# Optimization experiments

Hardware: AMD Instinct MI355X
Metric: run time of the kernel (lower is better)

Reference implementation:

```python
import jax, jax.numpy as jnp
import numpy as np

# 4D conv over (L, P, W, H) decomposed as k shifted 3D convs over (P, W, H),
# with the L spatial dim folded into the batch. Faithful to convNd(num_dims=4),
# stride 1, 'same' padding (padding = (k-1)//2), no bias.

def conv4d(x, w):
    # x: [B, C, L, P, W, H]; w: [O, I, k, k, k, k]
    k = w.shape[2]
    p = (k - 1) // 2
    B, C, L, P, Wd, Hd = x.shape
    O = w.shape[0]
    xp = jnp.pad(x, ((0, 0), (0, 0), (p, p), (0, 0), (0, 0), (0, 0)))
    dn = ('NCDHW', 'OIDHW', 'NCDHW')
    out = jnp.zeros((B, O, L, P, Wd, Hd), x.dtype)
    for dl in range(k):  # k <= 3, static loop over kernel taps along L
        xs = xp[:, :, dl:dl + L]                                  # [B,C,L,P,W,H]
        xs = xs.transpose(0, 2, 1, 3, 4, 5).reshape(B * L, C, P, Wd, Hd)
        y = jax.lax.conv_general_dilated(xs, w[:, :, dl], (1, 1, 1),
                                         [(p, p)] * 3, dimension_numbers=dn)
        out = out + y.reshape(B, L, O, P, Wd, Hd).transpose(0, 2, 1, 3, 4, 5)
    return out


def inception4d(x, weights):
    # mean over parallel 4D convs with kernel sizes 1, 3, ... (2i+1)
    acc = conv4d(x, weights[0])
    for w in weights[1:]:
        acc = acc + conv4d(x, w)
    return acc / len(weights)


def setup_inputs() -> dict:
    key = jax.random.key(0)
    ks = jax.random.split(key, 5)
    B, T, W, H, C = 4, 48, 8, 8, 32
    d_model, d_ff = 32, 64
    x = jax.random.normal(ks[0], (B, T, W, H, C), dtype=jnp.float32)
    # Inception_Block4D weights: kernel sizes 1 and 3 (num_kernels=2), no bias
    w1_0 = jax.random.normal(ks[1], (d_ff, d_model, 1, 1, 1, 1), dtype=jnp.float32) * 0.1
    w1_1 = jax.random.normal(ks[2], (d_ff, d_model, 3, 3, 3, 3), dtype=jnp.float32) * 0.02
    w2_0 = jax.random.normal(ks[3], (d_model, d_ff, 1, 1, 1, 1), dtype=jnp.float32) * 0.1
    w2_1 = jax.random.normal(ks[4], (d_model, d_ff, 3, 3, 3, 3), dtype=jnp.float32) * 0.02
    return {"x": x, "w1_0": w1_0, "w1_1": w1_1, "w2_0": w2_0, "w2_1": w2_1}


def reference(x, w1_0, w1_1, w2_0, w2_1):
    B, T, W, H, C = x.shape
    periods = (2, 3, 4)                       # FFT_for_Period hardcoded output
    xf = jnp.ones((B, len(periods)), x.dtype) # hardcoded uniform weights
    real_len = T                              # seq_len + pred_len
    res = []
    for period in periods:
        if real_len % period != 0:
            length = (real_len // period + 1) * period
            out = jnp.concatenate([x, x[:, -(length - real_len):]], axis=1)
        else:
            length = real_len
            out = x
        # [B, L, P, W, H, C] -> [B, C, L, P, W, H]
        out = out.reshape(B, length // period, period, W, H, C).transpose(0, 5, 1, 2, 3, 4)
        h = inception4d(out, [w1_0, w1_1])
        h = jax.nn.gelu(h, approximate=False)  # torch nn.GELU default (exact)
        h = inception4d(h, [w2_0, w2_1])
        # [B, C, L, P, W, H] -> [B, (L P), W, H, C]
        h = h.transpose(0, 2, 3, 4, 5, 1).reshape(B, length, W, H, C)
        res.append(h[:, :real_len])
    res = jnp.stack(res, axis=1)              # [B, k, T, W, H, C]
    pw = jax.nn.softmax(xf, axis=1).reshape(B, len(periods), 1, 1, 1, 1)
    return jnp.sum(res * pw, axis=1) + x
```

## Files before the change

### kernel.cpp

```cpp
#include <hip/hip_runtime.h>
#include <math.h>


typedef __attribute__((ext_vector_type(8))) short bf16x8;
typedef __attribute__((ext_vector_type(4))) float f32x4;
typedef unsigned short u16;

#define XC 3200
#define HC 6400
#define XSEG 617600
#define ZSEG_END 636800
#define W1OFF 636800
#define W2OFF 802688
#define H1OFF 968576
#define H1P 1235200
#define PREP_N 1300352
#define OUT_Q 98304
#define PREP_TOT (PREP_N + OUT_Q)

#define WAITVM(N) asm volatile("s_waitcnt vmcnt(" #N ")" ::: "memory")
#define SBAR()    asm volatile("s_barrier" ::: "memory")

__device__ __forceinline__ u16 f2bf(float f) {
    unsigned u = __float_as_uint(f);
    unsigned r = u + 0x7fffu + ((u >> 16) & 1u);
    return (u16)(r >> 16);
}
__device__ __forceinline__ float gelu_exact(float v) {
    return 0.5f * v * (1.0f + erff(v * 0.7071067811865476f));
}

__device__ __forceinline__ void cp1k(const u16* g, u16* l, int lane) {
    __builtin_amdgcn_global_load_lds(
        (const __attribute__((address_space(1))) unsigned int*)(g + lane * 8),
        (__attribute__((address_space(3))) unsigned int*)(l + lane * 8),
        16, 0, 0);
}

__global__ __launch_bounds__(256) void prep(
    const float* __restrict__ x,
    const float* __restrict__ w1_0, const float* __restrict__ w1_1,
    const float* __restrict__ w2_0, const float* __restrict__ w2_1,
    u16* __restrict__ ws, float* __restrict__ out) {
    int i = blockIdx.x * 256 + threadIdx.x;
    if (i < XSEG) {
        int cellidx = i / XC; int inner = i - cellidx * XC;
        int cellpos = inner >> 5; int low = inner & 31;
        int sc = low >> 3, jj = low & 7;
        int c = ((sc ^ (cellpos & 3)) << 3) + jj;
        int wp = cellpos / 10, hp = cellpos - (cellpos / 10) * 10;
        float v = 0.f;
        if (cellidx < 192 && wp >= 1 && wp <= 8 && hp >= 1 && hp <= 8)
            v = x[(cellidx * 64 + (wp - 1) * 8 + (hp - 1)) * 32 + c];
        ws[i] = f2bf(v);
    } else if (i < ZSEG_END) {
        int j = i - XSEG;
        int per = j / HC; int off = j - per * HC;
        ws[H1OFF + per * H1P + 192 * HC + off] = 0;
    } else if (i < ZSEG_END + 165888) {
        int j = i - W1OFF;
        int tap = j >> 11; int r = j & 2047;
        int chunk = r >> 3, jj = r & 7;
        int m = chunk & 15, nt = (chunk >> 4) & 3, quad = chunk >> 6;
        int o = nt * 16 + m, c = quad * 8 + jj;
        float v = 0.5f * w1_1[(o * 32 + c) * 81 + tap];
        if (tap == 40) v += 0.5f * w1_0[o * 32 + c];
        ws[i] = f2bf(v);
    } else if (i < PREP_N) {
        int j = i - W2OFF;
        int tap = j >> 11; int r = j & 2047;
        int chunk = r >> 3, jj = r & 7;
        int m = chunk & 15, nt = (chunk >> 4) & 1;
        int quad = (chunk >> 5) & 3, ks = chunk >> 7;
        int o = nt * 16 + m, c = ks * 32 + quad * 8 + jj;
        float v = 0.5f * w2_1[(o * 64 + c) * 81 + tap];
        if (tap == 40) v += 0.5f * w2_0[o * 64 + c];
        ws[i] = f2bf(v);
    } else if (i < PREP_TOT) {
        int j = i - PREP_N;
        ((float4*)out)[j] = ((const float4*)x)[j];
    }
}

template<int P>
__device__ __forceinline__ int cidx(int bb, int l2, int q2) {
    constexpr int L = 48 / P;
    return ((unsigned)l2 < (unsigned)L && (unsigned)q2 < (unsigned)P)
               ? bb * 48 + l2 * P + q2 : 192;
}

template<int P>
__device__ __forceinline__ void conv1_body(
    const u16* __restrict__ xs, const u16* __restrict__ w1b,
    u16* __restrict__ h1, int tp, int bb,
    u16* __restrict__ s_w, u16* __restrict__ s_a) {
    constexpr int HB = (P == 2) ? 0 : (P == 3) ? H1P : 2 * H1P;

    int tid = threadIdx.x;
    int lane = tid & 63, wv = tid >> 6;
    int m = lane & 15, quad = lane >> 4;
    int tloc = wv >> 1, nh = wv & 1;

    int t0 = tp * 2, t1 = tp * 2 + 1;
    int l0 = t0 / P, q0 = t0 - l0 * P;
    int l1 = t1 / P, q1 = t1 - l1 * P;

    int sp[4];
#pragma unroll
    for (int mt = 0; mt < 4; ++mt) {
        int pos = mt * 16 + m;
        sp[mt] = (pos >> 3) * 10 + (pos & 7);
    }

    f32x4 acc[4][2];
#pragma unroll
    for (int mt = 0; mt < 4; ++mt)
#pragma unroll
        for (int nt = 0; nt < 2; ++nt) acc[mt][nt] = f32x4{0.f, 0.f, 0.f, 0.f};

    auto stageW = [&](int cgn) {
        const u16* src = w1b + (cgn * 3) * 2048;
        u16* dst = s_w + (cgn & 3) * 6144;
        int p0 = wv * 3;
#pragma unroll
        for (int i = 0; i < 3; ++i)
            cp1k(src + (p0 + i) * 512, dst + (p0 + i) * 512, lane);
    };
    auto stageA = [&](int gg) {
        int dl = gg / 3, dq = gg - (gg / 3) * 3;
        const u16* c0 = xs + cidx<P>(bb, l0 + dl - 1, q0 + dq - 1) * XC;
        const u16* c1 = xs + cidx<P>(bb, l1 + dl - 1, q1 + dq - 1) * XC;
#pragma unroll
        for (int i = 0; i < 4; ++i) {
            int k = wv * 4 + i; if (k >= 14) k = 13;
            int cell = k / 7, pc = k - (k / 7) * 7;
            cp1k((cell ? c1 : c0) + pc * 512,
                 s_a + (cell * 2 + (gg & 1)) * 3584 + pc * 512, lane);
        }
    };

    stageW(0); stageA(0); stageW(1);

#pragma unroll 1
    for (int cg = 0; cg < 27; ++cg) {
        if (cg < 25) {
            stageW(cg + 2);
            if ((cg + 2) % 3 == 0) stageA((cg + 2) / 3);
        }
        if (cg == 25) { WAITVM(3); }
        else if (cg == 26) { WAITVM(0); }
        else if (cg % 3 == 0) { WAITVM(6); }
        else { WAITVM(10); }
        SBAR();

        int grp = cg / 3, part = cg - grp * 3;
        const u16* bw = s_w + (cg & 3) * 6144;
        const u16* ba = s_a + (tloc * 2 + (grp & 1)) * 3584;
        int dwb = part * 10;
#pragma unroll
        for (int j = 0; j < 3; ++j) {
            const u16* tw = bw + j * 2048;
            bf16x8 wf[2];
#pragma unroll
            for (int nt = 0; nt < 2; ++nt)
                wf[nt] = *(const bf16x8*)(tw +
                    (((quad * 4 + nh * 2 + nt) * 16 + m) << 3));
            bf16x8 af[4];
#pragma unroll
            for (int mt = 0; mt < 4; ++mt) {
                int cellpos = sp[mt] + dwb + j;
                af[mt] = *(const bf16x8*)(ba + cellpos * 32 +
                                          ((quad ^ (cellpos & 3)) << 3));
            }
#pragma unroll
            for (int mt = 0; mt < 4; ++mt)
#pragma unroll
                for (int nt = 0; nt < 2; ++nt)
                    acc[mt][nt] = __builtin_amdgcn_mfma_f32_16x16x32_bf16(
                        af[mt], wf[nt], acc[mt][nt], 0, 0, 0);
        }
    }

    int t = tp * 2 + tloc;
    u16* hcell = h1 + HB + (bb * 48 + t) * HC;
#pragma unroll
    for (int mt = 0; mt < 4; ++mt)
#pragma unroll
        for (int r = 0; r < 4; ++r) {
            int pos = mt * 16 + quad * 4 + r;
            int cellpos = ((pos >> 3) + 1) * 10 + (pos & 7) + 1;
#pragma unroll
            for (int nt = 0; nt < 2; ++nt) {
                int o = nh * 32 + nt * 16 + m;
                hcell[cellpos * 64 + (((o >> 3) ^ (cellpos & 7)) << 3) + (o & 7)] =
                    f2bf(gelu_exact(acc[mt][nt][r]));
            }
        }
    unsigned int* h32 = (unsigned int*)hcell;
#pragma unroll
    for (int it = 0; it < 18; ++it) {
        int k = it * 64 + lane;
        int bp = k >> 5, u = k & 31;
        int cp;
        if (bp < 10) cp = bp;
        else if (bp < 20) cp = 90 + (bp - 10);
        else if (bp < 28) cp = (bp - 19) * 10;
        else cp = (bp - 27) * 10 + 9;
        h32[cp * 32 + u] = 0;
    }
}

__global__ __launch_bounds__(256) void conv1_k(
    const u16* __restrict__ ws_x, const u16* __restrict__ ws_w1,
    u16* __restrict__ ws_h1) {
    __shared__ __align__(16) u16 s_w[4 * 6144];
    __shared__ __align__(16) u16 s_a[4 * 3584];
    int g = blockIdx.x;
    int jid = (g & 7) * 36 + (g >> 3);
    int per = jid / 96; int rem = jid - per * 96;
    int bb = rem / 24; int tp = rem - bb * 24;
    if (per == 0)      conv1_body<2>(ws_x, ws_w1, ws_h1, tp, bb, s_w, s_a);
    else if (per == 1) conv1_body<3>(ws_x, ws_w1, ws_h1, tp, bb, s_w, s_a);
    else               conv1_body<4>(ws_x, ws_w1, ws_h1, tp, bb, s_w, s_a);
}

template<int P>
__device__ __forceinline__ void conv2_body(
    const u16* __restrict__ h1, const u16* __restrict__ w2b,
    float* __restrict__ out, int tp, int bb,
    u16* __restrict__ s_w, u16* __restrict__ s_a) {
    constexpr int HB = (P == 2) ? 0 : (P == 3) ? H1P : 2 * H1P;

    int tid = threadIdx.x;
    int lane = tid & 63, wv = tid >> 6;
    int m = lane & 15, quad = lane >> 4;
    int tloc = wv >> 1, mh = wv & 1;

    int t0 = tp * 2, t1 = tp * 2 + 1;
    int l0 = t0 / P, q0 = t0 - l0 * P;
    int l1 = t1 / P, q1 = t1 - l1 * P;
    const u16* hb = h1 + HB;

    int sp[2];
#pragma unroll
    for (int mt = 0; mt < 2; ++mt) {
        int pos = mh * 32 + mt * 16 + m;
        sp[mt] = (pos >> 3) * 10 + (pos & 7);
    }

    f32x4 acc[2][2];
#pragma unroll
    for (int mt = 0; mt < 2; ++mt)
#pragma unroll
        for (int nt = 0; nt < 2; ++nt) acc[mt][nt] = f32x4{0.f, 0.f, 0.f, 0.f};

    auto stageW = [&](int cgn) {
        const u16* src = w2b + (cgn * 3) * 2048;
        u16* dst = s_w + (cgn & 1) * 6144;
        int p0 = wv * 3;
#pragma unroll
        for (int i = 0; i < 3; ++i)
            cp1k(src + (p0 + i) * 512, dst + (p0 + i) * 512, lane);
    };
    auto stageA = [&](int gg, int k0, int k1) {
        int dl = gg / 3, dq = gg - (gg / 3) * 3;
        const u16* c0 = hb + cidx<P>(bb, l0 + dl - 1, q0 + dq - 1) * HC;
        const u16* c1 = hb + cidx<P>(bb, l1 + dl - 1, q1 + dq - 1) * HC;
        for (int k = k0 + wv; k < k1; k += 4) {
            int cell = k / 13, pc = k - (k / 13) * 13;
            cp1k((cell ? c1 : c0) + pc * 512,
                 s_a + (cell * 2 + (gg & 1)) * 6656 + pc * 512, lane);
        }
    };

    stageW(0);
    stageA(0, 0, 26);

#pragma unroll 1
    for (int cg = 0; cg < 27; ++cg) {
        __syncthreads();
        if (cg < 26) stageW(cg + 1);
        int grp = cg / 3, part = cg - grp * 3;
        if (grp < 8) stageA(grp + 1, part * 9, (part == 2) ? 26 : part * 9 + 9);

        const u16* bw = s_w + (cg & 1) * 6144;
        const u16* ba = s_a + (tloc * 2 + (grp & 1)) * 6656;
        int dwb = part * 10;
#pragma unroll
        for (int j = 0; j < 3; ++j) {
            const u16* tw = bw + j * 2048;
            bf16x8 wf[2][2];
#pragma unroll
            for (int nt = 0; nt < 2; ++nt)
#pragma unroll
                for (int ks = 0; ks < 2; ++ks)
                    wf[nt][ks] = *(const bf16x8*)(tw +
                        ((((ks * 4 + quad) * 2 + nt) * 16 + m) << 3));
            bf16x8 af[2][2];
#pragma unroll
            for (int mt = 0; mt < 2; ++mt) {
                int cellpos = sp[mt] + dwb + j;
#pragma unroll
                for (int ks = 0; ks < 2; ++ks)
                    af[mt][ks] = *(const bf16x8*)(ba + cellpos * 64 +
                        (((ks * 4 + quad) ^ (cellpos & 7)) << 3));
            }
#pragma unroll
            for (int mt = 0; mt < 2; ++mt)
#pragma unroll
                for (int ks = 0; ks < 2; ++ks)
#pragma unroll
                    for (int nt = 0; nt < 2; ++nt)
                        acc[mt][nt] = __builtin_amdgcn_mfma_f32_16x16x32_bf16(
                            af[mt][ks], wf[nt][ks], acc[mt][nt], 0, 0, 0);
        }
    }

    int t = tp * 2 + tloc;
    float* orow = out + (bb * 48 + t) * 2048;
    const float s = 1.0f / 3.0f;
#pragma unroll
    for (int mt = 0; mt < 2; ++mt)
#pragma unroll
        for (int nt = 0; nt < 2; ++nt)
#pragma unroll
            for (int r = 0; r < 4; ++r) {
                int pos = mh * 32 + mt * 16 + quad * 4 + r;
                atomicAdd(&orow[pos * 32 + nt * 16 + m], acc[mt][nt][r] * s);
            }
}

__global__ __launch_bounds__(256) void conv2_k(
    const u16* __restrict__ ws_h1, const u16* __restrict__ ws_w2,
    float* __restrict__ out) {
    __shared__ __align__(16) u16 s_w[2 * 6144];
    __shared__ __align__(16) u16 s_a[4 * 6656];
    int g = blockIdx.x;
    int jid = (g & 7) * 36 + (g >> 3);
    int per = jid / 96; int rem = jid - per * 96;
    int bb = rem / 24; int tp = rem - bb * 24;
    if (per == 0)      conv2_body<2>(ws_h1, ws_w2, out, tp, bb, s_w, s_a);
    else if (per == 1) conv2_body<3>(ws_h1, ws_w2, out, tp, bb, s_w, s_a);
    else               conv2_body<4>(ws_h1, ws_w2, out, tp, bb, s_w, s_a);
}

extern "C" void kernel_launch(void* const* d_in, const int* in_sizes, int n_in,
                              void* d_out, int out_size, void* d_ws, size_t ws_size,
                              hipStream_t stream) {
    const float* x    = (const float*)d_in[0];
    const float* w1_0 = (const float*)d_in[1];
    const float* w1_1 = (const float*)d_in[2];
    const float* w2_0 = (const float*)d_in[3];
    const float* w2_1 = (const float*)d_in[4];
    float* out = (float*)d_out;

    u16* ws = (u16*)d_ws;
    u16* ws_x  = ws;
    u16* ws_w1 = ws + W1OFF;
    u16* ws_w2 = ws + W2OFF;
    u16* ws_h1 = ws + H1OFF;

    prep<<<(PREP_TOT + 255) / 256, 256, 0, stream>>>(
        x, w1_0, w1_1, w2_0, w2_1, ws, out);
    conv1_k<<<288, 256, 0, stream>>>(ws_x, ws_w1, ws_h1);
    conv2_k<<<288, 256, 0, stream>>>(ws_h1, ws_w2, out);
}
```

Before: 129.4 us.

## Split conv channels across two blocks and double grid size

Conv1 now gives each block half of the output channels, and conv2 gives each block half of the input channels, with partial sums combined through the existing atomic adds. The grid doubles to 576 blocks to fill the CUs better. The h1 intermediate is stored as two padded 32-channel halves per cell, and the weight packing is reordered to match. Conv2 also switches to the deeper 4-stage global_load_lds pipeline used by conv1. Both kernels gain occupancy hints. In exchange, every block re-stages the full activation tiles for its half, and conv2 issues twice as many atomic adds to the output.

```diff
diff --git a/kernel.cpp b/kernel.cpp
--- a/kernel.cpp
+++ b/kernel.cpp
@@ -7,14 +7,14 @@
 typedef unsigned short u16;
 
 #define XC 3200
-#define HC 6400
+#define HC2 7168
 #define XSEG 617600
-#define ZSEG_END 636800
-#define W1OFF 636800
-#define W2OFF 802688
-#define H1OFF 968576
-#define H1P 1235200
-#define PREP_N 1300352
+#define ZSEG_END 639104
+#define W1OFF 639104
+#define W2OFF 804992
+#define H1OFF 970880
+#define H1P 1383424
+#define PREP_N 970880
 #define OUT_Q 98304
 #define PREP_TOT (PREP_N + OUT_Q)
 
@@ -55,24 +55,25 @@
         ws[i] = f2bf(v);
     } else if (i < ZSEG_END) {
         int j = i - XSEG;
-        int per = j / HC; int off = j - per * HC;
-        ws[H1OFF + per * H1P + 192 * HC + off] = 0;
-    } else if (i < ZSEG_END + 165888) {
+        int per = j / 7168; int off = j - per * 7168;
+        ws[H1OFF + per * H1P + 192 * 7168 + off] = 0;
+    } else if (i < W2OFF) {
         int j = i - W1OFF;
         int tap = j >> 11; int r = j & 2047;
-        int chunk = r >> 3, jj = r & 7;
-        int m = chunk & 15, nt = (chunk >> 4) & 3, quad = chunk >> 6;
-        int o = nt * 16 + m, c = quad * 8 + jj;
+        int nh = r >> 10; int rr = r & 1023;
+        int chunkh = rr >> 3, jj = rr & 7;
+        int m = chunkh & 15, nq = (chunkh >> 4) & 1, quad = chunkh >> 5;
+        int o = nh * 32 + nq * 16 + m, c = quad * 8 + jj;
         float v = 0.5f * w1_1[(o * 32 + c) * 81 + tap];
         if (tap == 40) v += 0.5f * w1_0[o * 32 + c];
         ws[i] = f2bf(v);
     } else if (i < PREP_N) {
         int j = i - W2OFF;
         int tap = j >> 11; int r = j & 2047;
-        int chunk = r >> 3, jj = r & 7;
-        int m = chunk & 15, nt = (chunk >> 4) & 1;
-        int quad = (chunk >> 5) & 3, ks = chunk >> 7;
-        int o = nt * 16 + m, c = ks * 32 + quad * 8 + jj;
+        int kh = r >> 10; int rr = r & 1023;
+        int chunkh = rr >> 3, jj = rr & 7;
+        int m = chunkh & 15, nt = (chunkh >> 4) & 1, quad = chunkh >> 5;
+        int o = nt * 16 + m, c = kh * 32 + quad * 8 + jj;
         float v = 0.5f * w2_1[(o * 64 + c) * 81 + tap];
         if (tap == 40) v += 0.5f * w2_0[o * 64 + c];
         ws[i] = f2bf(v);
@@ -92,39 +93,40 @@
 template<int P>
 __device__ __forceinline__ void conv1_body(
     const u16* __restrict__ xs, const u16* __restrict__ w1b,
-    u16* __restrict__ h1, int tp, int bb,
+    u16* __restrict__ h1, int tp, int bb, int nh,
     u16* __restrict__ s_w, u16* __restrict__ s_a) {
     constexpr int HB = (P == 2) ? 0 : (P == 3) ? H1P : 2 * H1P;
 
     int tid = threadIdx.x;
     int lane = tid & 63, wv = tid >> 6;
     int m = lane & 15, quad = lane >> 4;
-    int tloc = wv >> 1, nh = wv & 1;
+    int tloc = wv >> 1, mh = wv & 1;
 
     int t0 = tp * 2, t1 = tp * 2 + 1;
     int l0 = t0 / P, q0 = t0 - l0 * P;
     int l1 = t1 / P, q1 = t1 - l1 * P;
 
-    int sp[4];
-#pragma unroll
-    for (int mt = 0; mt < 4; ++mt) {
-        int pos = mt * 16 + m;
-        sp[mt] = (pos >> 3) * 10 + (pos & 7);
-    }
-
-    f32x4 acc[4][2];
-#pragma unroll
-    for (int mt = 0; mt < 4; ++mt)
-#pragma unroll
-        for (int nt = 0; nt < 2; ++nt) acc[mt][nt] = f32x4{0.f, 0.f, 0.f, 0.f};
+    int sp[2];
+#pragma unroll
+    for (int mtl = 0; mtl < 2; ++mtl) {
+        int pos = (mh * 2 + mtl) * 16 + m;
+        sp[mtl] = (pos >> 3) * 10 + (pos & 7);
+    }
+
+    f32x4 acc[2][2];
+#pragma unroll
+    for (int mtl = 0; mtl < 2; ++mtl)
+#pragma unroll
+        for (int nq = 0; nq < 2; ++nq) acc[mtl][nq] = f32x4{0.f, 0.f, 0.f, 0.f};
 
     auto stageW = [&](int cgn) {
-        const u16* src = w1b + (cgn * 3) * 2048;
-        u16* dst = s_w + (cgn & 3) * 6144;
-        int p0 = wv * 3;
-#pragma unroll
-        for (int i = 0; i < 3; ++i)
-            cp1k(src + (p0 + i) * 512, dst + (p0 + i) * 512, lane);
+        const u16* src = w1b + (cgn * 3) * 2048 + nh * 1024;
+        u16* dst = s_w + (cgn & 3) * 3072;
+#pragma unroll
+        for (int i = 0; i < 2; ++i) {
+            int k = wv * 2 + i; if (k >= 6) k = 5;
+            cp1k(src + (k >> 1) * 2048 + (k & 1) * 512, dst + k * 512, lane);
+        }
     };
     auto stageA = [&](int gg) {
         int dl = gg / 3, dq = gg - (gg / 3) * 3;
@@ -147,87 +149,91 @@
             stageW(cg + 2);
             if ((cg + 2) % 3 == 0) stageA((cg + 2) / 3);
         }
-        if (cg == 25) { WAITVM(3); }
+        if (cg == 25) { WAITVM(2); }
         else if (cg == 26) { WAITVM(0); }
-        else if (cg % 3 == 0) { WAITVM(6); }
-        else { WAITVM(10); }
+        else if (cg % 3 == 0) { WAITVM(4); }
+        else { WAITVM(8); }
         SBAR();
 
         int grp = cg / 3, part = cg - grp * 3;
-        const u16* bw = s_w + (cg & 3) * 6144;
+        const u16* bw = s_w + (cg & 3) * 3072;
         const u16* ba = s_a + (tloc * 2 + (grp & 1)) * 3584;
         int dwb = part * 10;
 #pragma unroll
         for (int j = 0; j < 3; ++j) {
-            const u16* tw = bw + j * 2048;
+            const u16* tw = bw + j * 1024;
             bf16x8 wf[2];
 #pragma unroll
-            for (int nt = 0; nt < 2; ++nt)
-                wf[nt] = *(const bf16x8*)(tw +
-                    (((quad * 4 + nh * 2 + nt) * 16 + m) << 3));
-            bf16x8 af[4];
-#pragma unroll
-            for (int mt = 0; mt < 4; ++mt) {
-                int cellpos = sp[mt] + dwb + j;
-                af[mt] = *(const bf16x8*)(ba + cellpos * 32 +
-                                          ((quad ^ (cellpos & 3)) << 3));
+            for (int nq = 0; nq < 2; ++nq)
+                wf[nq] = *(const bf16x8*)(tw + (((quad * 2 + nq) * 16 + m) << 3));
+            bf16x8 af[2];
+#pragma unroll
+            for (int mtl = 0; mtl < 2; ++mtl) {
+                int cellpos = sp[mtl] + dwb + j;
+                af[mtl] = *(const bf16x8*)(ba + cellpos * 32 +
+                                           ((quad ^ (cellpos & 3)) << 3));
             }
 #pragma unroll
-            for (int mt = 0; mt < 4; ++mt)
-#pragma unroll
-                for (int nt = 0; nt < 2; ++nt)
-                    acc[mt][nt] = __builtin_amdgcn_mfma_f32_16x16x32_bf16(
-                        af[mt], wf[nt], acc[mt][nt], 0, 0, 0);
+            for (int mtl = 0; mtl < 2; ++mtl)
+#pragma unroll
+                for (int nq = 0; nq < 2; ++nq)
+                    acc[mtl][nq] = __builtin_amdgcn_mfma_f32_16x16x32_bf16(
+                        af[mtl], wf[nq], acc[mtl][nq], 0, 0, 0);
         }
     }
 
     int t = tp * 2 + tloc;
-    u16* hcell = h1 + HB + (bb * 48 + t) * HC;
-#pragma unroll
-    for (int mt = 0; mt < 4; ++mt)
+    u16* hh = h1 + HB + (bb * 48 + t) * HC2 + nh * 3584;
+#pragma unroll
+    for (int mtl = 0; mtl < 2; ++mtl)
 #pragma unroll
         for (int r = 0; r < 4; ++r) {
-            int pos = mt * 16 + quad * 4 + r;
+            int pos = (mh * 2 + mtl) * 16 + quad * 4 + r;
             int cellpos = ((pos >> 3) + 1) * 10 + (pos & 7) + 1;
 #pragma unroll
-            for (int nt = 0; nt < 2; ++nt) {
-                int o = nh * 32 + nt * 16 + m;
-                hcell[cellpos * 64 + (((o >> 3) ^ (cellpos & 7)) << 3) + (o & 7)] =
-                    f2bf(gelu_exact(acc[mt][nt][r]));
+            for (int nq = 0; nq < 2; ++nq) {
+                int ol = nq * 16 + m;
+                hh[cellpos * 32 + (((ol >> 3) ^ (cellpos & 3)) << 3) + (ol & 7)] =
+                    f2bf(gelu_exact(acc[mtl][nq][r]));
             }
         }
-    unsigned int* h32 = (unsigned int*)hcell;
-#pragma unroll
-    for (int it = 0; it < 18; ++it) {
-        int k = it * 64 + lane;
-        int bp = k >> 5, u = k & 31;
-        int cp;
-        if (bp < 10) cp = bp;
-        else if (bp < 20) cp = 90 + (bp - 10);
-        else if (bp < 28) cp = (bp - 19) * 10;
-        else cp = (bp - 27) * 10 + 9;
-        h32[cp * 32 + u] = 0;
-    }
-}
-
-__global__ __launch_bounds__(256) void conv1_k(
+#pragma unroll
+    for (int it = 0; it < 5; ++it) {
+        int k = it * 256 + tid;
+        if (k < 1152) {
+            int tb = k >= 576; int rr = k - tb * 576;
+            int bp = rr >> 4, u = rr & 15;
+            int cp;
+            if (bp < 10) cp = bp;
+            else if (bp < 20) cp = 90 + (bp - 10);
+            else if (bp < 28) cp = (bp - 19) * 10;
+            else cp = (bp - 27) * 10 + 9;
+            unsigned int* h32 = (unsigned int*)(h1 + HB +
+                (bb * 48 + tp * 2 + tb) * HC2 + nh * 3584);
+            h32[cp * 16 + u] = 0;
+        }
+    }
+}
+
+__global__ __launch_bounds__(256, 3) void conv1_k(
     const u16* __restrict__ ws_x, const u16* __restrict__ ws_w1,
     u16* __restrict__ ws_h1) {
-    __shared__ __align__(16) u16 s_w[4 * 6144];
+    __shared__ __align__(16) u16 s_w[4 * 3072];
     __shared__ __align__(16) u16 s_a[4 * 3584];
     int g = blockIdx.x;
-    int jid = (g & 7) * 36 + (g >> 3);
-    int per = jid / 96; int rem = jid - per * 96;
-    int bb = rem / 24; int tp = rem - bb * 24;
-    if (per == 0)      conv1_body<2>(ws_x, ws_w1, ws_h1, tp, bb, s_w, s_a);
-    else if (per == 1) conv1_body<3>(ws_x, ws_w1, ws_h1, tp, bb, s_w, s_a);
-    else               conv1_body<4>(ws_x, ws_w1, ws_h1, tp, bb, s_w, s_a);
+    int jid = (g & 7) * 72 + (g >> 3);
+    int per = jid / 192; int rem = jid - per * 192;
+    int bb = rem / 48; int r2 = rem - bb * 48;
+    int tp = r2 >> 1, nh = r2 & 1;
+    if (per == 0)      conv1_body<2>(ws_x, ws_w1, ws_h1, tp, bb, nh, s_w, s_a);
+    else if (per == 1) conv1_body<3>(ws_x, ws_w1, ws_h1, tp, bb, nh, s_w, s_a);
+    else               conv1_body<4>(ws_x, ws_w1, ws_h1, tp, bb, nh, s_w, s_a);
 }
 
 template<int P>
 __device__ __forceinline__ void conv2_body(
     const u16* __restrict__ h1, const u16* __restrict__ w2b,
-    float* __restrict__ out, int tp, int bb,
+    float* __restrict__ out, int tp, int bb, int kh,
     u16* __restrict__ s_w, u16* __restrict__ s_a) {
     constexpr int HB = (P == 2) ? 0 : (P == 3) ? H1P : 2 * H1P;
 
@@ -243,76 +249,77 @@
 
     int sp[2];
 #pragma unroll
-    for (int mt = 0; mt < 2; ++mt) {
-        int pos = mh * 32 + mt * 16 + m;
-        sp[mt] = (pos >> 3) * 10 + (pos & 7);
+    for (int mtl = 0; mtl < 2; ++mtl) {
+        int pos = (mh * 2 + mtl) * 16 + m;
+        sp[mtl] = (pos >> 3) * 10 + (pos & 7);
     }
 
     f32x4 acc[2][2];
 #pragma unroll
-    for (int mt = 0; mt < 2; ++mt)
-#pragma unroll
-        for (int nt = 0; nt < 2; ++nt) acc[mt][nt] = f32x4{0.f, 0.f, 0.f, 0.f};
+    for (int mtl = 0; mtl < 2; ++mtl)
+#pragma unroll
+        for (int nt = 0; nt < 2; ++nt) acc[mtl][nt] = f32x4{0.f, 0.f, 0.f, 0.f};
 
     auto stageW = [&](int cgn) {
-        const u16* src = w2b + (cgn * 3) * 2048;
-        u16* dst = s_w + (cgn & 1) * 6144;
-        int p0 = wv * 3;
-#pragma unroll
-        for (int i = 0; i < 3; ++i)
-            cp1k(src + (p0 + i) * 512, dst + (p0 + i) * 512, lane);
+        const u16* src = w2b + (cgn * 3) * 2048 + kh * 1024;
+        u16* dst = s_w + (cgn & 3) * 3072;
+#pragma unroll
+        for (int i = 0; i < 2; ++i) {
+            int k = wv * 2 + i; if (k >= 6) k = 5;
+            cp1k(src + (k >> 1) * 2048 + (k & 1) * 512, dst + k * 512, lane);
+        }
     };
-    auto stageA = [&](int gg, int k0, int k1) {
+    auto stageA = [&](int gg) {
         int dl = gg / 3, dq = gg - (gg / 3) * 3;
-        const u16* c0 = hb + cidx<P>(bb, l0 + dl - 1, q0 + dq - 1) * HC;
-        const u16* c1 = hb + cidx<P>(bb, l1 + dl - 1, q1 + dq - 1) * HC;
-        for (int k = k0 + wv; k < k1; k += 4) {
-            int cell = k / 13, pc = k - (k / 13) * 13;
+        const u16* c0 = hb + cidx<P>(bb, l0 + dl - 1, q0 + dq - 1) * HC2 + kh * 3584;
+        const u16* c1 = hb + cidx<P>(bb, l1 + dl - 1, q1 + dq - 1) * HC2 + kh * 3584;
+#pragma unroll
+        for (int i = 0; i < 4; ++i) {
+            int k = wv * 4 + i; if (k >= 14) k = 13;
+            int cell = k / 7, pc = k - (k / 7) * 7;
             cp1k((cell ? c1 : c0) + pc * 512,
-                 s_a + (cell * 2 + (gg & 1)) * 6656 + pc * 512, lane);
+                 s_a + (cell * 2 + (gg & 1)) * 3584 + pc * 512, lane);
         }
     };
 
-    stageW(0);
-    stageA(0, 0, 26);
+    stageW(0); stageA(0); stageW(1);
 
 #pragma unroll 1
     for (int cg = 0; cg < 27; ++cg) {
-        __syncthreads();
-        if (cg < 26) stageW(cg + 1);
+        if (cg < 25) {
+            stageW(cg + 2);
+            if ((cg + 2) % 3 == 0) stageA((cg + 2) / 3);
+        }
+        if (cg == 25) { WAITVM(2); }
+        else if (cg == 26) { WAITVM(0); }
+        else if (cg % 3 == 0) { WAITVM(4); }
+        else { WAITVM(8); }
+        SBAR();
+
         int grp = cg / 3, part = cg - grp * 3;
-        if (grp < 8) stageA(grp + 1, part * 9, (part == 2) ? 26 : part * 9 + 9);
-
-        const u16* bw = s_w + (cg & 1) * 6144;
-        const u16* ba = s_a + (tloc * 2 + (grp & 1)) * 6656;
+        const u16* bw = s_w + (cg & 3) * 3072;
+        const u16* ba = s_a + (tloc * 2 + (grp & 1)) * 3584;
         int dwb = part * 10;
 #pragma unroll
         for (int j = 0; j < 3; ++j) {
-            const u16* tw = bw + j * 2048;
-            bf16x8 wf[2][2];
+            const u16* tw = bw + j * 1024;
+            bf16x8 wf[2];
 #pragma unroll
             for (int nt = 0; nt < 2; ++nt)
-#pragma unroll
-                for (int ks = 0; ks < 2; ++ks)
-                    wf[nt][ks] = *(const bf16x8*)(tw +
-                        ((((ks * 4 + quad) * 2 + nt) * 16 + m) << 3));
-            bf16x8 af[2][2];
-#pragma unroll
-            for (int mt = 0; mt < 2; ++mt) {
-                int cellpos = sp[mt] + dwb + j;
-#pragma unroll
-                for (int ks = 0; ks < 2; ++ks)
-                    af[mt][ks] = *(const bf16x8*)(ba + cellpos * 64 +
-                        (((ks * 4 + quad) ^ (cellpos & 7)) << 3));
+                wf[nt] = *(const bf16x8*)(tw + (((quad * 2 + nt) * 16 + m) << 3));
+            bf16x8 af[2];
+#pragma unroll
+            for (int mtl = 0; mtl < 2; ++mtl) {
+                int cellpos = sp[mtl] + dwb + j;
+                af[mtl] = *(const bf16x8*)(ba + cellpos * 32 +
+                                           ((quad ^ (cellpos & 3)) << 3));
             }
 #pragma unroll
-            for (int mt = 0; mt < 2; ++mt)
-#pragma unroll
-                for (int ks = 0; ks < 2; ++ks)
-#pragma unroll
-                    for (int nt = 0; nt < 2; ++nt)
-                        acc[mt][nt] = __builtin_amdgcn_mfma_f32_16x16x32_bf16(
-                            af[mt][ks], wf[nt][ks], acc[mt][nt], 0, 0, 0);
+            for (int mtl = 0; mtl < 2; ++mtl)
+#pragma unroll
+                for (int nt = 0; nt < 2; ++nt)
+                    acc[mtl][nt] = __builtin_amdgcn_mfma_f32_16x16x32_bf16(
+                        af[mtl], wf[nt], acc[mtl][nt], 0, 0, 0);
         }
     }
 
@@ -320,28 +327,29 @@
     float* orow = out + (bb * 48 + t) * 2048;
     const float s = 1.0f / 3.0f;
 #pragma unroll
-    for (int mt = 0; mt < 2; ++mt)
+    for (int mtl = 0; mtl < 2; ++mtl)
 #pragma unroll
         for (int nt = 0; nt < 2; ++nt)
 #pragma unroll
             for (int r = 0; r < 4; ++r) {
-                int pos = mh * 32 + mt * 16 + quad * 4 + r;
-                atomicAdd(&orow[pos * 32 + nt * 16 + m], acc[mt][nt][r] * s);
+                int pos = (mh * 2 + mtl) * 16 + quad * 4 + r;
+                atomicAdd(&orow[pos * 32 + nt * 16 + m], acc[mtl][nt][r] * s);
             }
 }
 
-__global__ __launch_bounds__(256) void conv2_k(
+__global__ __launch_bounds__(256, 3) void conv2_k(
     const u16* __restrict__ ws_h1, const u16* __restrict__ ws_w2,
     float* __restrict__ out) {
-    __shared__ __align__(16) u16 s_w[2 * 6144];
-    __shared__ __align__(16) u16 s_a[4 * 6656];
+    __shared__ __align__(16) u16 s_w[4 * 3072];
+    __shared__ __align__(16) u16 s_a[4 * 3584];
     int g = blockIdx.x;
-    int jid = (g & 7) * 36 + (g >> 3);
-    int per = jid / 96; int rem = jid - per * 96;
-    int bb = rem / 24; int tp = rem - bb * 24;
-    if (per == 0)      conv2_body<2>(ws_h1, ws_w2, out, tp, bb, s_w, s_a);
-    else if (per == 1) conv2_body<3>(ws_h1, ws_w2, out, tp, bb, s_w, s_a);
-    else               conv2_body<4>(ws_h1, ws_w2, out, tp, bb, s_w, s_a);
+    int jid = (g & 7) * 72 + (g >> 3);
+    int per = jid / 192; int rem = jid - per * 192;
+    int bb = rem / 48; int r2 = rem - bb * 48;
+    int tp = r2 >> 1, kh = r2 & 1;
+    if (per == 0)      conv2_body<2>(ws_h1, ws_w2, out, tp, bb, kh, s_w, s_a);
+    else if (per == 1) conv2_body<3>(ws_h1, ws_w2, out, tp, bb, kh, s_w, s_a);
+    else               conv2_body<4>(ws_h1, ws_w2, out, tp, bb, kh, s_w, s_a);
 }
 
 extern "C" void kernel_launch(void* const* d_in, const int* in_sizes, int n_in,
@@ -362,6 +370,6 @@
 
     prep<<<(PREP_TOT + 255) / 256, 256, 0, stream>>>(
         x, w1_0, w1_1, w2_0, w2_1, ws, out);
-    conv1_k<<<288, 256, 0, stream>>>(ws_x, ws_w1, ws_h1);
-    conv2_k<<<288, 256, 0, stream>>>(ws_h1, ws_w2, out);
-}
+    conv1_k<<<576, 256, 0, stream>>>(ws_x, ws_w1, ws_h1);
+    conv2_k<<<576, 256, 0, stream>>>(ws_h1, ws_w2, out);
+}
```

Result: faster. 120.1 us (-7.2%).
